# Kernel optimization log

Measured on AMD Instinct MI355X. Metric: run time of the kernel, lower is better.

Reference implementation:

```python
import jax, jax.numpy as jnp
import numpy as np
import math

N_WIRES = 8
DIM = 2 ** N_WIRES  # 256

# Pauli-Z sign table: wire 0 is the most-significant axis of the statevector.
_idx = np.arange(DIM)
_SIGNS = np.stack([1.0 - 2.0 * ((_idx >> (N_WIRES - 1 - w)) & 1) for w in range(N_WIRES)], axis=1).astype(np.float32)  # [256, 8]


def _cnot(state, c, t):
    # state: [N, 2, 2, ..., 2]; flip target axis where control bit == 1
    s0, s1 = jnp.split(state, 2, axis=1 + c)
    s1 = jnp.flip(s1, axis=1 + t)
    return jnp.concatenate([s0, s1], axis=1 + c)


def _quantum_heads(x, theta):
    """Simulate the QLayer circuit. x: [N, 8] -> PauliZ expectations [N, 8].

    Circuit: RX(x_i) then RX(theta_i) on wire i (commute -> RX(x_i+theta_i)),
    CNOT chain (0,1)...(6,7),(7,0), MeasureAll(PauliZ).
    """
    phi = 0.5 * (x + theta)  # RX half-angle
    c = jnp.cos(phi)
    s = jnp.sin(phi)
    # RX(a)|0> = cos(a/2)|0> - i sin(a/2)|1>
    amps = jax.lax.complex(jnp.stack([c, jnp.zeros_like(c)], axis=-1),
                           jnp.stack([jnp.zeros_like(s), -s], axis=-1))  # [N, 8, 2] complex64
    # Product state as rank-8 tensor [N, 2, ..., 2]
    state = amps[:, 0]
    for w in range(1, N_WIRES):
        state = state[..., None] * amps[:, w].reshape((-1,) + (1,) * w + (2,))
    # Entangling CNOT ring
    for w in range(N_WIRES - 1):
        state = _cnot(state, w, w + 1)
    state = _cnot(state, N_WIRES - 1, 0)
    probs = jnp.abs(state.reshape(-1, DIM)) ** 2  # [N, 256]
    return probs @ jnp.asarray(_SIGNS)  # [N, 8]


def setup_inputs() -> dict:
    key = jax.random.key(0)
    k1, k2, k3, k4 = jax.random.split(key, 4)
    B, S, E = 32, 512, 64
    return {
        "x": jax.random.normal(k1, (B, S, E), dtype=jnp.float32),
        "theta": jax.random.normal(k2, (N_WIRES,), dtype=jnp.float32),
        "W": jax.random.normal(k3, (E, E), dtype=jnp.float32) * 0.05,
        "b": jax.random.normal(k4, (E,), dtype=jnp.float32) * 0.05,
    }


def reference(x, theta, W, b):
    B, S, E = x.shape
    H = E // N_WIRES  # num_heads
    # q = k = v: same deterministic quantum projection applied to the same x.
    z = _quantum_heads(x.reshape(B * S * H, N_WIRES), theta).reshape(B, S, H, N_WIRES)
    scale = 1.0 / math.sqrt(E // H)
    # NOTE: matmul over last dims -> attention across heads within each token.
    scores = jnp.einsum('bshd,bstd->bsht', z, z) * scale  # [B, S, H, H]
    attn = jax.nn.softmax(scores, axis=-1)
    out = jnp.einsum('bsht,bstd->bshd', attn, z).reshape(B, S, E)
    return out @ W.T + b
```

## Files before the change

kernel.cpp:

```cpp
#include <hip/hip_runtime.h>


#define TOK_PER_BLK 32

__global__ __launch_bounds__(256, 2)
void mhaq_fused2(const float* __restrict__ x,
                 const float* __restrict__ theta,
                 const float* __restrict__ W,
                 const float* __restrict__ bias,
                 float* __restrict__ out,
                 int n_tokens)
{
    __shared__ __align__(16) float Ws[64 * 64];
    __shared__ __align__(16) float bs[64];
    __shared__ __align__(16) float zs[TOK_PER_BLK * 68];
    __shared__ __align__(16) float os[TOK_PER_BLK * 68];

    const int tid = threadIdx.x;
    const int tl  = tid >> 3;
    const int g   = tid & 7;
    const int token = blockIdx.x * TOK_PER_BLK + tl;
    const bool valid = token < n_tokens;

    {
        const float4* __restrict__ Wv = reinterpret_cast<const float4*>(W);
        float4* Ws4 = reinterpret_cast<float4*>(Ws);
        #pragma unroll
        for (int i = 0; i < 4; ++i) {
            int idx = i * 256 + tid;
            int j   = idx >> 4;
            int k4  = idx & 15;
            Ws4[(j << 4) | (k4 ^ ((j >> 3) & 7))] = Wv[idx];
        }
        if (tid < 16)
            reinterpret_cast<float4*>(bs)[tid] =
                reinterpret_cast<const float4*>(bias)[tid];
    }

    float zh[8];
    {
        float4 a = make_float4(0.f, 0.f, 0.f, 0.f);
        float4 b4 = make_float4(0.f, 0.f, 0.f, 0.f);
        if (valid) {
            const float4* __restrict__ xp =
                reinterpret_cast<const float4*>(x) + (size_t)token * 16 + g * 2;
            a = xp[0]; b4 = xp[1];
        }
        float c0 = __cosf(a.x  + theta[0]);
        float c1 = __cosf(a.y  + theta[1]);
        float c2 = __cosf(a.z  + theta[2]);
        float c3 = __cosf(a.w  + theta[3]);
        float c4 = __cosf(b4.x + theta[4]);
        float c5 = __cosf(b4.y + theta[5]);
        float c6 = __cosf(b4.z + theta[6]);
        float c7 = __cosf(b4.w + theta[7]);
        float p1 = c0 * c1;
        float p2 = p1 * c2;
        float p3 = p2 * c3;
        float p4 = p3 * c4;
        float p5 = p4 * c5;
        float p6 = p5 * c6;
        float p7 = p6 * c7;
        float s6 = c6 * c7;
        float s5 = c5 * s6;
        float s4 = c4 * s5;
        float s3 = c3 * s4;
        float s2 = c2 * s3;
        float s1 = c1 * s2;
        zh[0] = s1; zh[1] = p1; zh[2] = p2; zh[3] = p3;
        zh[4] = p4; zh[5] = p5; zh[6] = p6; zh[7] = p7;

        float4* z4 = reinterpret_cast<float4*>(zs) + tl * 17 + g * 2;
        z4[0] = make_float4(zh[0], zh[1], zh[2], zh[3]);
        z4[1] = make_float4(zh[4], zh[5], zh[6], zh[7]);
    }
    __syncthreads();

    {
        __align__(16) float zf[64];
        const float4* z4 = reinterpret_cast<const float4*>(zs) + tl * 17;
        #pragma unroll
        for (int k4 = 0; k4 < 16; ++k4)
            *reinterpret_cast<float4*>(&zf[4 * k4]) = z4[k4];

        const float scale = 0.35355339059327373f;
        float sc[8];
        float m = -4.0f;
        #pragma unroll
        for (int t = 0; t < 8; ++t) {
            float s = 0.f;
            #pragma unroll
            for (int d = 0; d < 8; ++d)
                s = fmaf(zh[d], zf[t * 8 + d], s);
            s *= scale;
            sc[t] = s;
            m = fmaxf(m, s);
        }
        float sum = 0.f;
        #pragma unroll
        for (int t = 0; t < 8; ++t) {
            sc[t] = __expf(sc[t] - m);
            sum += sc[t];
        }
        float inv = 1.0f / sum;

        float oh[8];
        #pragma unroll
        for (int d = 0; d < 8; ++d) {
            float acc = 0.f;
            #pragma unroll
            for (int t = 0; t < 8; ++t)
                acc = fmaf(sc[t], zf[t * 8 + d], acc);
            oh[d] = acc * inv;
        }
        float4* o4 = reinterpret_cast<float4*>(os) + tl * 17 + g * 2;
        o4[0] = make_float4(oh[0], oh[1], oh[2], oh[3]);
        o4[1] = make_float4(oh[4], oh[5], oh[6], oh[7]);
    }
    __syncthreads();

    {
        __align__(16) float of[64];
        const float4* o4 = reinterpret_cast<const float4*>(os) + tl * 17;
        #pragma unroll
        for (int k4 = 0; k4 < 16; ++k4)
            *reinterpret_cast<float4*>(&of[4 * k4]) = o4[k4];

        float acc[8];
        #pragma unroll
        for (int jj = 0; jj < 8; ++jj)
            acc[jj] = bs[g * 8 + jj];

        const float4* Ws4 = reinterpret_cast<const float4*>(Ws);
        #pragma unroll
        for (int k4 = 0; k4 < 16; ++k4) {
            float4 ov = *reinterpret_cast<const float4*>(&of[4 * k4]);
            #pragma unroll
            for (int jj = 0; jj < 8; ++jj) {
                int j = g * 8 + jj;
                float4 w4 = Ws4[(j << 4) | (k4 ^ g)];
                acc[jj] = fmaf(ov.x, w4.x, acc[jj]);
                acc[jj] = fmaf(ov.y, w4.y, acc[jj]);
                acc[jj] = fmaf(ov.z, w4.z, acc[jj]);
                acc[jj] = fmaf(ov.w, w4.w, acc[jj]);
            }
        }

        if (valid) {
            float4* yout = reinterpret_cast<float4*>(out) + (size_t)token * 16 + g * 2;
            yout[0] = make_float4(acc[0], acc[1], acc[2], acc[3]);
            yout[1] = make_float4(acc[4], acc[5], acc[6], acc[7]);
        }
    }
}

extern "C" void kernel_launch(void* const* d_in, const int* in_sizes, int n_in,
                              void* d_out, int out_size, void* d_ws, size_t ws_size,
                              hipStream_t stream)
{
    const float* x     = (const float*)d_in[0];
    const float* theta = (const float*)d_in[1];
    const float* W     = (const float*)d_in[2];
    const float* b     = (const float*)d_in[3];
    float* out         = (float*)d_out;

    const int n_tokens = in_sizes[0] / 64;
    const int blocks   = (n_tokens + TOK_PER_BLK - 1) / TOK_PER_BLK;
    mhaq_fused2<<<blocks, 256, 0, stream>>>(x, theta, W, b, out, n_tokens);
}
```

Baseline: 11.40 us.

## Run output projection on bf16 MFMA with bf16 W and attention outputs

The output projection (32 tokens x 64 by 64x64 W per block) now runs on the 16x16x32 bf16 MFMA instruction instead of per-thread FP32 FMAs. W and the attention outputs are rounded to bf16 and stored in padded LDS rows, which also halves LDS traffic for the projection. Results are written as scalar stores in MFMA output layout rather than float4 per token. The tradeoff is reduced precision from bf16 rounding of both operands, plus less coalesced output stores.

```diff
diff --git a/kernel.cpp b/kernel.cpp
--- a/kernel.cpp
+++ b/kernel.cpp
@@ -3,18 +3,27 @@
 
 #define TOK_PER_BLK 32
 
+typedef __attribute__((ext_vector_type(8))) short short8;
+typedef __attribute__((ext_vector_type(4))) float f32x4;
+
+__device__ inline unsigned short f2bf(float f) {
+    unsigned u = __float_as_uint(f);
+    u += 0x7FFF + ((u >> 16) & 1);
+    return (unsigned short)(u >> 16);
+}
+
 __global__ __launch_bounds__(256, 2)
-void mhaq_fused2(const float* __restrict__ x,
+void mhaq_fused3(const float* __restrict__ x,
                  const float* __restrict__ theta,
                  const float* __restrict__ W,
                  const float* __restrict__ bias,
                  float* __restrict__ out,
                  int n_tokens)
 {
-    __shared__ __align__(16) float Ws[64 * 64];
-    __shared__ __align__(16) float bs[64];
-    __shared__ __align__(16) float zs[TOK_PER_BLK * 68];
-    __shared__ __align__(16) float os[TOK_PER_BLK * 68];
+    __shared__ __align__(16) unsigned short Ws[64 * 72];
+    __shared__ __align__(16) float          zs[TOK_PER_BLK * 68];
+    __shared__ __align__(16) unsigned short os[TOK_PER_BLK * 72];
+    __shared__ float bs[64];
 
     const int tid = threadIdx.x;
     const int tl  = tid >> 3;
@@ -24,13 +33,14 @@
 
     {
         const float4* __restrict__ Wv = reinterpret_cast<const float4*>(W);
-        float4* Ws4 = reinterpret_cast<float4*>(Ws);
         #pragma unroll
         for (int i = 0; i < 4; ++i) {
             int idx = i * 256 + tid;
             int j   = idx >> 4;
-            int k4  = idx & 15;
-            Ws4[(j << 4) | (k4 ^ ((j >> 3) & 7))] = Wv[idx];
+            int c4  = idx & 15;
+            float4 w = Wv[idx];
+            *reinterpret_cast<ushort4*>(&Ws[j * 72 + c4 * 4]) =
+                make_ushort4(f2bf(w.x), f2bf(w.y), f2bf(w.z), f2bf(w.w));
         }
         if (tid < 16)
             reinterpret_cast<float4*>(bs)[tid] =
@@ -39,7 +49,7 @@
 
     float zh[8];
     {
-        float4 a = make_float4(0.f, 0.f, 0.f, 0.f);
+        float4 a  = make_float4(0.f, 0.f, 0.f, 0.f);
         float4 b4 = make_float4(0.f, 0.f, 0.f, 0.f);
         if (valid) {
             const float4* __restrict__ xp =
@@ -70,7 +80,7 @@
         zh[0] = s1; zh[1] = p1; zh[2] = p2; zh[3] = p3;
         zh[4] = p4; zh[5] = p5; zh[6] = p6; zh[7] = p7;
 
-        float4* z4 = reinterpret_cast<float4*>(zs) + tl * 17 + g * 2;
+        float4* z4 = reinterpret_cast<float4*>(zs + tl * 68 + g * 8);
         z4[0] = make_float4(zh[0], zh[1], zh[2], zh[3]);
         z4[1] = make_float4(zh[4], zh[5], zh[6], zh[7]);
     }
@@ -78,10 +88,11 @@
 
     {
         __align__(16) float zf[64];
-        const float4* z4 = reinterpret_cast<const float4*>(zs) + tl * 17;
+        const float* zrow = zs + tl * 68;
         #pragma unroll
         for (int k4 = 0; k4 < 16; ++k4)
-            *reinterpret_cast<float4*>(&zf[4 * k4]) = z4[k4];
+            *reinterpret_cast<float4*>(&zf[4 * k4]) =
+                *reinterpret_cast<const float4*>(&zrow[4 * k4]);
 
         const float scale = 0.35355339059327373f;
         float sc[8];
@@ -104,52 +115,59 @@
         }
         float inv = 1.0f / sum;
 
-        float oh[8];
+        unsigned short oh[8];
         #pragma unroll
         for (int d = 0; d < 8; ++d) {
             float acc = 0.f;
             #pragma unroll
             for (int t = 0; t < 8; ++t)
                 acc = fmaf(sc[t], zf[t * 8 + d], acc);
-            oh[d] = acc * inv;
+            oh[d] = f2bf(acc * inv);
         }
-        float4* o4 = reinterpret_cast<float4*>(os) + tl * 17 + g * 2;
-        o4[0] = make_float4(oh[0], oh[1], oh[2], oh[3]);
-        o4[1] = make_float4(oh[4], oh[5], oh[6], oh[7]);
+        ushort4* o4 = reinterpret_cast<ushort4*>(&os[tl * 72 + g * 8]);
+        o4[0] = make_ushort4(oh[0], oh[1], oh[2], oh[3]);
+        o4[1] = make_ushort4(oh[4], oh[5], oh[6], oh[7]);
     }
     __syncthreads();
 
     {
-        __align__(16) float of[64];
-        const float4* o4 = reinterpret_cast<const float4*>(os) + tl * 17;
+        const int lane = tid & 63;
+        const int wave = tid >> 6;
+        const int mt   = wave & 1;
+        const int np   = wave >> 1;
+        const int lr   = lane & 15;
+        const int lg   = lane >> 4;
+
+        short8 bfrag[2][2];
         #pragma unroll
-        for (int k4 = 0; k4 < 16; ++k4)
-            *reinterpret_cast<float4*>(&of[4 * k4]) = o4[k4];
+        for (int nt = 0; nt < 2; ++nt) {
+            int j = np * 32 + nt * 16 + lr;
+            #pragma unroll
+            for (int kt = 0; kt < 2; ++kt)
+                bfrag[nt][kt] = *reinterpret_cast<const short8*>(
+                    &Ws[j * 72 + kt * 32 + lg * 8]);
+        }
+        short8 afrag[2];
+        #pragma unroll
+        for (int kt = 0; kt < 2; ++kt)
+            afrag[kt] = *reinterpret_cast<const short8*>(
+                &os[(mt * 16 + lr) * 72 + kt * 32 + lg * 8]);
 
-        float acc[8];
         #pragma unroll
-        for (int jj = 0; jj < 8; ++jj)
-            acc[jj] = bs[g * 8 + jj];
-
-        const float4* Ws4 = reinterpret_cast<const float4*>(Ws);
-        #pragma unroll
-        for (int k4 = 0; k4 < 16; ++k4) {
-            float4 ov = *reinterpret_cast<const float4*>(&of[4 * k4]);
+        for (int nt = 0; nt < 2; ++nt) {
+            int j = np * 32 + nt * 16 + lr;
+            float bj = bs[j];
+            f32x4 acc = {bj, bj, bj, bj};
             #pragma unroll
-            for (int jj = 0; jj < 8; ++jj) {
-                int j = g * 8 + jj;
-                float4 w4 = Ws4[(j << 4) | (k4 ^ g)];
-                acc[jj] = fmaf(ov.x, w4.x, acc[jj]);
-                acc[jj] = fmaf(ov.y, w4.y, acc[jj]);
-                acc[jj] = fmaf(ov.z, w4.z, acc[jj]);
-                acc[jj] = fmaf(ov.w, w4.w, acc[jj]);
+            for (int kt = 0; kt < 2; ++kt)
+                acc = __builtin_amdgcn_mfma_f32_16x16x32_bf16(
+                    afrag[kt], bfrag[nt][kt], acc, 0, 0, 0);
+            #pragma unroll
+            for (int r = 0; r < 4; ++r) {
+                int trow = blockIdx.x * TOK_PER_BLK + mt * 16 + lg * 4 + r;
+                if (trow < n_tokens)
+                    out[(size_t)trow * 64 + j] = acc[r];
             }
-        }
-
-        if (valid) {
-            float4* yout = reinterpret_cast<float4*>(out) + (size_t)token * 16 + g * 2;
-            yout[0] = make_float4(acc[0], acc[1], acc[2], acc[3]);
-            yout[1] = make_float4(acc[4], acc[5], acc[6], acc[7]);
         }
     }
 }
@@ -166,5 +184,5 @@
 
     const int n_tokens = in_sizes[0] / 64;
     const int blocks   = (n_tokens + TOK_PER_BLK - 1) / TOK_PER_BLK;
-    mhaq_fused2<<<blocks, 256, 0, stream>>>(x, theta, W, b, out, n_tokens);
+    mhaq_fused3<<<blocks, 256, 0, stream>>>(x, theta, W, b, out, n_tokens);
 }
```

Result: faster. 9.805 us (-14.0%).
